# Kernel tuning notes

Measured on AMD Instinct MI355X. Metric: run time of the kernel, lower is better.

The kernel has to match this reference:

```python
import jax, jax.numpy as jnp
import numpy as np

DIM, H, D, B, L = 1024, 8, 64, 1, 256


def silu(v):
    return v * jax.nn.sigmoid(v)


def setup_inputs() -> dict:
    key = jax.random.key(0)
    ks = jax.random.split(key, 12)
    n = lambda i, shape, scale=1.0: jax.random.normal(ks[i], shape, dtype=jnp.float32) * scale
    return {
        "x": n(0, (B, L, DIM)),
        "hidden_real": n(1, (B, H, D)),
        "hidden_imag": n(2, (B, H, D)),
        "w_in1": n(3, (DIM, DIM), 1.0 / np.sqrt(DIM)),
        "b_in1": jnp.zeros((DIM,), jnp.float32),
        "w_in2": n(4, (DIM, H * D * 4), 1.0 / np.sqrt(DIM)),
        "b_in2": jnp.zeros((H * D * 4,), jnp.float32),
        "w_out1": n(5, (H * D * 2, DIM), 1.0 / np.sqrt(H * D * 2)),
        "b_out1": jnp.zeros((DIM,), jnp.float32),
        "w_out2": n(6, (DIM, DIM), 1.0 / np.sqrt(DIM)),
        "b_out2": jnp.zeros((DIM,), jnp.float32),
        "mat_v_real": n(7, (H, D, D)),
        "mat_v_imag": n(8, (H, D, D)),
    }


def reference(x, hidden_real, hidden_imag, w_in1, b_in1, w_in2, b_in2,
              w_out1, b_out1, w_out2, b_out2, mat_v_real, mat_v_imag):
    batch, slen, _ = x.shape
    t = silu(x @ w_in1 + b_in1)
    t = t @ w_in2 + b_in2                       # (B, L, 4*H*D)
    z = t.reshape(batch, slen, H, D, 2, 2)      # [..., {x,a}, {re,im}]
    xc = jax.lax.complex(z[..., 0, 0], z[..., 0, 1])   # (B, L, H, D) complex
    ac = jax.lax.complex(z[..., 1, 0], z[..., 1, 1])

    # normalize a: unit phase * sigmoid(log(|a|^2)) magnitude
    mag2 = ac.real * ac.real + ac.imag * ac.imag
    ac = ac * (jax.lax.rsqrt(mag2) * jax.nn.sigmoid(jnp.log(mag2)))

    a_ln = jnp.log(ac)                          # (B, L, H, D) complex
    al = jnp.transpose(a_ln, (0, 2, 3, 1))      # (B, H, D, L)

    # triu-broadcast + cumsum along cols == the FFT conv-with-ones in the original
    idx = jnp.arange(slen)
    triu = idx[:, None] <= idx[None, :]          # row i, col j: keep j >= i
    tri = jnp.where(triu, al[..., None, :], 0.0)  # (B, H, D, L, L)
    cum = jnp.cumsum(tri, axis=-1)               # cum[i, k] = sum_{j=i..k} a_ln[j]
    keep = (idx[:, None] - 1) <= idx[None, :]    # triu(diagonal=-1)
    c = jnp.where(keep, jnp.exp(cum), 0.0)       # c[i,k] = prod_{j=i..k} a[j]; c[i,i-1]=1

    V = jax.lax.complex(mat_v_real, mat_v_imag)  # (H, D, D)
    Vinv = jnp.linalg.inv(V)
    hidden = jax.lax.complex(hidden_real, hidden_imag)  # (B, H, D)

    x_roll = jnp.concatenate([hidden.astype(xc.dtype)[:, None], xc[:, :-1]], axis=1)
    u = jnp.einsum('hno,blho->blhn', Vinv, x_roll)       # V^{-1} applied per head
    h = jnp.einsum('bholm,blho->bmho', c, u)             # banded product-scan
    h = h.at[:, -1].add(jnp.einsum('hno,bho->bhn', Vinv, xc[:, -1]))
    h = jnp.einsum('hno,blho->blhn', V, h)               # back to V-basis

    hidden_next = h[:, -1]                                # (B, H, D) complex
    hr = jnp.stack([h.real, h.imag], axis=-1).reshape(batch, slen, H * D * 2)
    y = silu(hr @ w_out1 + b_out1)
    y = y @ w_out2 + b_out2
    return y, hidden_next
```

## Files before the change

kernel.cpp:

```cpp
#include <hip/hip_runtime.h>
#include <math.h>

#define DIMN 1024
#define NH 8
#define ND 64
#define LSEQ 256
#define HD 512

typedef __attribute__((ext_vector_type(8))) short short8;
typedef __attribute__((ext_vector_type(4))) float f32x4;

__device__ __forceinline__ float2 cmul(float2 a, float2 b){
    return make_float2(a.x*b.x - a.y*b.y, a.x*b.y + a.y*b.x);
}
__device__ __forceinline__ ushort f2bf(float f){
    union { float f; unsigned u; } v; v.f = f;
    unsigned r = v.u + 0x7FFF + ((v.u >> 16) & 1);
    return (ushort)(r >> 16);
}

#define ISTR 65
#define ASTR 40
#define BK 32

__device__ __forceinline__ void inv_gj_blocked(const float* __restrict__ Vr,
        const float* __restrict__ Vi, float2* __restrict__ Vinv,
        int h, int tid, float2* Mx){
    for (int idx = tid; idx < 4096; idx += 512){
        int i = idx >> 6, j = idx & 63;
        Mx[i*ISTR + j] = make_float2(Vr[h*4096 + idx], Vi[h*4096 + idx]);
    }
    __syncthreads();
    const int w = tid >> 6, l = tid & 63;
    const int rbase = w*8;
    for (int kb = 0; kb < 8; ++kb){
        const int k0 = kb*8;
        if (w == 0){
            float2 pr[8];
            #pragma unroll
            for (int m = 0; m < 8; ++m) pr[m] = Mx[l*ISTR + k0 + m];
            #pragma unroll
            for (int k = 0; k < 8; ++k){
                const int gk = k0 + k;
                float2 d; d.x = __shfl(pr[k].x, gk); d.y = __shfl(pr[k].y, gk);
                float im = 1.f/(d.x*d.x + d.y*d.y);
                float2 p = make_float2(d.x*im, -d.y*im);
                float2 spr[8];
                #pragma unroll
                for (int m = 0; m < 8; ++m){
                    float2 t; t.x = __shfl(pr[m].x, gk); t.y = __shfl(pr[m].y, gk);
                    spr[m] = (m == k) ? p : cmul(t, p);
                }
                float2 f = pr[k];
                if (l == gk){
                    #pragma unroll
                    for (int m = 0; m < 8; ++m) pr[m] = spr[m];
                } else {
                    #pragma unroll
                    for (int m = 0; m < 8; ++m){
                        float2 u = cmul(f, spr[m]);
                        if (m == k){ pr[m].x = -u.x;  pr[m].y = -u.y;  }
                        else       { pr[m].x -= u.x;  pr[m].y -= u.y;  }
                    }
                }
            }
            #pragma unroll
            for (int m = 0; m < 8; ++m) Mx[l*ISTR + k0 + m] = pr[m];
        }
        __syncthreads();
        float2 br[8];
        #pragma unroll
        for (int m = 0; m < 8; ++m) br[m] = Mx[(k0+m)*ISTR + l];
        __syncthreads();
        if (((unsigned)(l - k0)) >= 8u){
            #pragma unroll
            for (int rr = 0; rr < 8; ++rr){
                const int r = rbase + rr;
                float2 acc;
                if (((unsigned)(r - k0)) < 8u){ acc.x = 0.f; acc.y = 0.f; }
                else acc = Mx[r*ISTR + l];
                #pragma unroll
                for (int m = 0; m < 8; ++m){
                    float2 Pv = Mx[r*ISTR + k0 + m];
                    acc.x += Pv.x*br[m].x - Pv.y*br[m].y;
                    acc.y += Pv.x*br[m].y + Pv.y*br[m].x;
                }
                Mx[r*ISTR + l] = acc;
            }
        }
        __syncthreads();
    }
    for (int idx = tid; idx < 4096; idx += 512){
        int i = idx >> 6, j = idx & 63;
        Vinv[h*4096 + idx] = Mx[i*ISTR + j];
    }
}

__device__ __forceinline__ void w3eff_tile(const float* __restrict__ Vr,
        const float* __restrict__ Vi, const float* __restrict__ w3,
        ushort* __restrict__ W3bt, int t, int tid, float* lds){
    const int n0 = (t & 31)*32;
    const int c0 = (t >> 5)*32;
    const int h  = c0 >> 7;
    const int og0 = (c0 & 127) >> 1;
    float* Vbr = lds;
    float* Vbi = lds + 1024;
    float* Wb  = lds + 2048;
    for (int q = tid; q < 1024; q += 512){
        int dd = q >> 4, oo = q & 15;
        Vbr[q] = Vr[(h*64+dd)*64 + og0 + oo];
        Vbi[q] = Vi[(h*64+dd)*64 + og0 + oo];
    }
    for (int q = tid; q < 4096; q += 512){
        int row = q >> 5, nn = q & 31;
        Wb[q] = w3[(h*128 + row)*1024 + n0 + nn];
    }
    __syncthreads();
    const int nn = tid & 31, oo = tid >> 5;
    float ar = 0.f, ai = 0.f;
    #pragma unroll 8
    for (int dd = 0; dd < 64; ++dd){
        float vr = Vbr[dd*16 + oo], vi = Vbi[dd*16 + oo];
        float w0 = Wb[(dd*2)*32 + nn], w1v = Wb[(dd*2+1)*32 + nn];
        ar += vr*w0 + vi*w1v;
        ai += -vi*w0 + vr*w1v;
    }
    W3bt[(n0+nn)*1024 + c0 + oo*2 + 0] = f2bf(ar);
    W3bt[(n0+nn)*1024 + c0 + oo*2 + 1] = f2bf(ai);
}

__device__ __forceinline__ void gemm1_direct_tile(const float* __restrict__ x,
        const float* __restrict__ w1, const float* __restrict__ bias,
        ushort* __restrict__ Cb, int tile, int tid8, ushort* lds){
    ushort* As = lds;
    ushort* Bs = lds + 64*ASTR;
    const int bm = (tile & 3)*64, bn = (tile >> 2)*64;
    const int wave = tid8 >> 6, l = tid8 & 63;
    const int wr = (wave >> 1)*32, wc = (wave & 1)*32;
    const int ml = l & 15, quad = l >> 4;
    f32x4 acc[2][2];
    #pragma unroll
    for (int i=0;i<2;++i)
        #pragma unroll
        for (int j=0;j<2;++j) acc[i][j] = (f32x4){0.f,0.f,0.f,0.f};
    const int c0r = tid8 >> 2, c0s = tid8 & 3;
    const int bn_n = tid8 & 63, bk0 = (tid8 >> 6)*8;
    for (int k0 = 0; k0 < DIMN; k0 += BK){
        float4 a0 = *(const float4*)&x[(bm+c0r)*DIMN + k0 + c0s*8];
        float4 a1 = *(const float4*)&x[(bm+c0r)*DIMN + k0 + c0s*8 + 4];
        float bv[8];
        #pragma unroll
        for (int kk = 0; kk < 8; ++kk)
            bv[kk] = w1[(k0 + bk0 + kk)*DIMN + bn + bn_n];
        __syncthreads();
        ushort4 u0; u0.x=f2bf(a0.x); u0.y=f2bf(a0.y); u0.z=f2bf(a0.z); u0.w=f2bf(a0.w);
        ushort4 u1; u1.x=f2bf(a1.x); u1.y=f2bf(a1.y); u1.z=f2bf(a1.z); u1.w=f2bf(a1.w);
        *(ushort4*)&As[c0r*ASTR + c0s*8]     = u0;
        *(ushort4*)&As[c0r*ASTR + c0s*8 + 4] = u1;
        #pragma unroll
        for (int kk = 0; kk < 8; ++kk)
            Bs[bn_n*ASTR + bk0 + kk] = f2bf(bv[kk]);
        __syncthreads();
        short8 af[2], bfv[2];
        #pragma unroll
        for (int f=0; f<2; ++f){
            af[f]  = *(const short8*)&As[(wr + f*16 + ml)*ASTR + quad*8];
            bfv[f] = *(const short8*)&Bs[(wc + f*16 + ml)*ASTR + quad*8];
        }
        #pragma unroll
        for (int i=0;i<2;++i)
            #pragma unroll
            for (int j=0;j<2;++j)
                acc[i][j] = __builtin_amdgcn_mfma_f32_16x16x32_bf16(af[i], bfv[j], acc[i][j], 0,0,0);
    }
    #pragma unroll
    for (int i=0;i<2;++i){
        #pragma unroll
        for (int j=0;j<2;++j){
            const int gcol = bn + wc + j*16 + ml;
            const float bsv = bias[gcol];
            #pragma unroll
            for (int r=0;r<4;++r){
                const int grow = bm + wr + i*16 + quad*4 + r;
                float val = acc[i][j][r] + bsv;
                val *= 1.f/(1.f + expf(-val));
                Cb[grow*DIMN + gcol] = f2bf(val);
            }
        }
    }
}

__global__ __launch_bounds__(512) void mix1_kernel(
        const float* __restrict__ x,
        const float* __restrict__ w1, const float* __restrict__ w2,
        const float* __restrict__ w3, const float* __restrict__ w4,
        const float* __restrict__ Vr, const float* __restrict__ Vi,
        const float* __restrict__ b1,
        ushort* __restrict__ t1_bf,
        ushort* __restrict__ w2t, ushort* __restrict__ W3bt,
        ushort* __restrict__ w4t, float2* __restrict__ Vinv){
    __shared__ __align__(16) char lds_raw[33280];
    const int b = blockIdx.x;
    const int tid = threadIdx.x;
    const int half = tid >> 8;

    if (b < 32){
        gemm1_direct_tile(x, w1, b1, t1_bf, b*2 + half, tid & 255,
                          (ushort*)lds_raw + half*(128*ASTR));
        return;
    }
    if (b < 40){
        inv_gj_blocked(Vr, Vi, Vinv, b - 32, tid, (float2*)lds_raw);
        return;
    }
    int widx = b - 40;
    if (widx >= 1536){
        w3eff_tile(Vr, Vi, w3, W3bt, widx - 1536, tid, (float*)lds_raw);
        return;
    }
    const float* W; ushort* Wt; int K = 1024, N;
    if (widx < 1024){ W = w2; Wt = w2t; N = 2048; }
    else            { W = w4; Wt = w4t; N = 1024; widx -= 1024; }
    const int t = widx*2 + half;
    const int tiles_n = N >> 5;
    const int n0 = (t % tiles_n) * 32, k0 = (t / tiles_n) * 32;
    float* tile = (float*)lds_raw + half*(32*33);
    const int tx = tid & 31, ty = (tid >> 5) & 7;
    #pragma unroll
    for (int i = 0; i < 4; ++i)
        tile[(ty + i*8)*33 + tx] = W[(k0 + ty + i*8)*N + n0 + tx];
    __syncthreads();
    #pragma unroll
    for (int i = 0; i < 4; ++i){
        int r = ty + i*8;
        Wt[(n0 + r)*K + k0 + tx] = f2bf(tile[tx*33 + r]);
    }
}

__global__ __launch_bounds__(512) void inv_kernel(const float* __restrict__ Vr,
                                                  const float* __restrict__ Vi,
                                                  float2* __restrict__ Vinv){
    __shared__ float2 Mx[64*ISTR];
    inv_gj_blocked(Vr, Vi, Vinv, blockIdx.x, threadIdx.x, Mx);
}

__global__ __launch_bounds__(256) void transpose_cvt(const float* __restrict__ W,
                 ushort* __restrict__ Wt, int K, int N){
    __shared__ float tile[32][33];
    const int n0 = blockIdx.x * 32, k0 = blockIdx.y * 32;
    const int tx = threadIdx.x & 31, ty = threadIdx.x >> 5;
    #pragma unroll
    for (int i = 0; i < 4; ++i)
        tile[ty + i*8][tx] = W[(k0 + ty + i*8)*N + n0 + tx];
    __syncthreads();
    #pragma unroll
    for (int i = 0; i < 4; ++i){
        int r = ty + i*8;
        Wt[(n0 + r)*K + k0 + tx] = f2bf(tile[tx][r]);
    }
}

__global__ __launch_bounds__(256) void cvt_bf16_kernel(const float* __restrict__ in,
                                 ushort* __restrict__ o, int n4){
    int i = blockIdx.x*256 + threadIdx.x;
    if (i < n4){
        float4 v = ((const float4*)in)[i];
        ushort4 u; u.x=f2bf(v.x); u.y=f2bf(v.y); u.z=f2bf(v.z); u.w=f2bf(v.w);
        ((ushort4*)o)[i] = u;
    }
}

#define BM 64
#define BN 64
template<int ACT>
__global__ __launch_bounds__(256) void gemm_bt(const ushort* __restrict__ A,
                 const ushort* __restrict__ Bt, const float* __restrict__ bias,
                 float* __restrict__ Cf, ushort* __restrict__ Cb,
                 float2* __restrict__ XCo, float2* __restrict__ Ao,
                 int M, int N, int K,
                 const float* __restrict__ tVr, const float* __restrict__ tVi,
                 const float2* __restrict__ S255, float* __restrict__ out_tail,
                 int tail_n){
    __shared__ ushort As[BM*ASTR];
    __shared__ ushort Bs[BN*ASTR];
    const int tid = threadIdx.x;
    const int bm = blockIdx.y * BM, bn = blockIdx.x * BN;
    const int wave = tid >> 6, l = tid & 63;
    const int wr = (wave >> 1) * 32, wc = (wave & 1) * 32;
    const int ml = l & 15, quad = l >> 4;

    if (ACT == 0 && out_tail != nullptr && blockIdx.x == 0 && blockIdx.y == 0){
        for (int hn = tid; hn < 512; hn += 256){
            int h = hn >> 6;
            float2 acc2 = make_float2(0.f, 0.f);
            #pragma unroll 8
            for (int o = 0; o < 64; ++o){
                float2 v = make_float2(tVr[hn*64+o], tVi[hn*64+o]);
                float2 p = cmul(v, S255[h*64+o]);
                acc2.x += p.x; acc2.y += p.y;
            }
            if (tail_n >= 1024){
                out_tail[hn]       = acc2.x;
                out_tail[512 + hn] = acc2.y;
            } else if (tail_n >= 512){
                out_tail[hn] = acc2.x;
            }
        }
    }

    f32x4 acc[2][2];
    #pragma unroll
    for (int i=0;i<2;++i)
        #pragma unroll
        for (int j=0;j<2;++j) acc[i][j] = (f32x4){0.f,0.f,0.f,0.f};
    const int c0r = tid >> 2;
    const int c0s = tid & 3;
    for (int k0 = 0; k0 < K; k0 += BK){
        uint4 av = *(const uint4*)&A [(bm + c0r)*K + k0 + c0s*8];
        uint4 bv = *(const uint4*)&Bt[(bn + c0r)*K + k0 + c0s*8];
        __syncthreads();
        *(uint4*)&As[c0r*ASTR + c0s*8] = av;
        *(uint4*)&Bs[c0r*ASTR + c0s*8] = bv;
        __syncthreads();
        short8 af[2], bfv[2];
        #pragma unroll
        for (int f=0; f<2; ++f){
            af[f]  = *(const short8*)&As[(wr + f*16 + ml)*ASTR + quad*8];
            bfv[f] = *(const short8*)&Bs[(wc + f*16 + ml)*ASTR + quad*8];
        }
        #pragma unroll
        for (int i=0;i<2;++i)
            #pragma unroll
            for (int j=0;j<2;++j)
                acc[i][j] = __builtin_amdgcn_mfma_f32_16x16x32_bf16(af[i], bfv[j], acc[i][j], 0,0,0);
    }
    #pragma unroll
    for (int i=0;i<2;++i){
        #pragma unroll
        for (int j=0;j<2;++j){
            const int gcol = bn + wc + j*16 + ml;
            const float bsv = bias[gcol];
            #pragma unroll
            for (int r=0;r<4;++r){
                const int grow = bm + wr + i*16 + quad*4 + r;
                float val = acc[i][j][r] + bsv;
                if (ACT == 2){
                    float v1 = __shfl_down(val, 1);
                    float v2 = __shfl_down(val, 2);
                    float v3 = __shfl_down(val, 3);
                    if ((l & 3) == 0){
                        int hd = gcol >> 2;
                        XCo[grow*HD + hd] = make_float2(val, v1);
                        float m2 = v2*v2 + v3*v3;
                        float s = sqrtf(m2)/(1.f + m2);
                        Ao[grow*HD + hd] = make_float2(v2*s, v3*s);
                    }
                } else if (ACT == 1){
                    val *= 1.f/(1.f + expf(-val));
                    Cb[grow*N + gcol] = f2bf(val);
                } else {
                    Cf[grow*N + gcol] = val;
                }
            }
        }
    }
}

__global__ __launch_bounds__(512) void upscan_kernel(const float2* __restrict__ Vinv,
        const float* __restrict__ hidr, const float* __restrict__ him,
        const float2* __restrict__ XC, const float2* __restrict__ Aseq,
        ushort* __restrict__ Sb, float2* __restrict__ S255){
    __shared__ float4 buf[2][2][LSEQ];
    __shared__ float2 vrow[2][64];
    __shared__ float2 inu[2];
    const int b = blockIdx.x;
    const int tid = threadIdx.x;
    const int g = tid >> 8, m = tid & 255;
    const int hn = b*2 + g;
    const int h = hn >> 6;
    if (m < 64) vrow[g][m] = Vinv[hn*64 + m];
    __syncthreads();
    float2 acc = make_float2(0.f, 0.f);
    const float2* xrow = &XC[m*HD + h*64];
    #pragma unroll 8
    for (int o=0;o<64;++o){
        float2 p = cmul(vrow[g][o], xrow[o]);
        acc.x += p.x; acc.y += p.y;
    }
    if (m == 0){
        float2 i0 = make_float2(0.f, 0.f);
        #pragma unroll 8
        for (int o=0;o<64;++o){
            float2 hv = make_float2(hidr[h*64+o], him[h*64+o]);
            float2 p = cmul(vrow[g][o], hv);
            i0.x += p.x; i0.y += p.y;
        }
        inu[g] = i0;
    }
    float2 a = Aseq[m*HD + hn];
    buf[0][g][m] = make_float4(a.x, a.y, acc.x, acc.y);
    __syncthreads();
    int pb = 0;
    #pragma unroll
    for (int d = 1; d < LSEQ; d <<= 1){
        float4 cur = buf[pb][g][m];
        float4 o2 = cur;
        if (m >= d){
            float4 prev = buf[pb][g][m-d];
            float2 cA = make_float2(cur.x, cur.y), cU = make_float2(cur.z, cur.w);
            float2 pA = make_float2(prev.x, prev.y), pU = make_float2(prev.z, prev.w);
            float2 nA = cmul(cA, pA);
            float2 nU = cmul(cA, pU);
            nU.x += cU.x; nU.y += cU.y;
            o2 = make_float4(nA.x, nA.y, nU.x, nU.y);
        }
        buf[pb^1][g][m] = o2;
        pb ^= 1;
        __syncthreads();
    }
    float4 t = buf[pb][g][m];
    float2 init = inu[g];
    float2 st = cmul(make_float2(t.x, t.y), init);
    st.x += t.z; st.y += t.w;
    Sb[m*DIMN + hn*2]   = f2bf(st.x);
    Sb[m*DIMN + hn*2+1] = f2bf(st.y);
    if (m == LSEQ-1) S255[hn] = st;
}

__global__ __launch_bounds__(256) void vmul_kernel(const float* __restrict__ Vr,
                            const float* __restrict__ Vi,
                            const float2* __restrict__ S, ushort* __restrict__ hrb,
                            float* __restrict__ out_tail, int tail_n){
    int g = blockIdx.x*256 + threadIdx.x;
    int m = g >> 9, hn = g & 511;
    int h = hn >> 6;
    const float* vr = &Vr[hn*64];
    const float* vi = &Vi[hn*64];
    const float2* srow = &S[m*HD + h*64];
    float2 acc = make_float2(0.f, 0.f);
    #pragma unroll 8
    for (int o=0;o<64;++o){
        float2 v = make_float2(vr[o], vi[o]);
        float2 p = cmul(v, srow[o]);
        acc.x += p.x; acc.y += p.y;
    }
    hrb[m*DIMN + hn*2]   = f2bf(acc.x);
    hrb[m*DIMN + hn*2+1] = f2bf(acc.y);
    if (m == LSEQ-1){
        if (tail_n >= 1024){
            out_tail[hn]       = acc.x;
            out_tail[512 + hn] = acc.y;
        } else if (tail_n >= 512){
            out_tail[hn] = acc.x;
        }
    }
}

__global__ __launch_bounds__(512) void upscan_f32_kernel(const float2* __restrict__ Vinv,
        const float* __restrict__ hidr, const float* __restrict__ him,
        const float2* __restrict__ XC, const float2* __restrict__ Aseq,
        float2* __restrict__ S){
    __shared__ float4 buf[2][2][LSEQ];
    __shared__ float2 vrow[2][64];
    __shared__ float2 inu[2];
    const int b = blockIdx.x;
    const int tid = threadIdx.x;
    const int g = tid >> 8, m = tid & 255;
    const int hn = b*2 + g;
    const int h = hn >> 6;
    if (m < 64) vrow[g][m] = Vinv[hn*64 + m];
    __syncthreads();
    float2 acc = make_float2(0.f, 0.f);
    const float2* xrow = &XC[m*HD + h*64];
    #pragma unroll 8
    for (int o=0;o<64;++o){
        float2 p = cmul(vrow[g][o], xrow[o]);
        acc.x += p.x; acc.y += p.y;
    }
    if (m == 0){
        float2 i0 = make_float2(0.f, 0.f);
        #pragma unroll 8
        for (int o=0;o<64;++o){
            float2 hv = make_float2(hidr[h*64+o], him[h*64+o]);
            float2 p = cmul(vrow[g][o], hv);
            i0.x += p.x; i0.y += p.y;
        }
        inu[g] = i0;
    }
    float2 a = Aseq[m*HD + hn];
    buf[0][g][m] = make_float4(a.x, a.y, acc.x, acc.y);
    __syncthreads();
    int pb = 0;
    #pragma unroll
    for (int d = 1; d < LSEQ; d <<= 1){
        float4 cur = buf[pb][g][m];
        float4 o2 = cur;
        if (m >= d){
            float4 prev = buf[pb][g][m-d];
            float2 cA = make_float2(cur.x, cur.y), cU = make_float2(cur.z, cur.w);
            float2 pA = make_float2(prev.x, prev.y), pU = make_float2(prev.z, prev.w);
            float2 nA = cmul(cA, pA);
            float2 nU = cmul(cA, pU);
            nU.x += cU.x; nU.y += cU.y;
            o2 = make_float4(nA.x, nA.y, nU.x, nU.y);
        }
        buf[pb^1][g][m] = o2;
        pb ^= 1;
        __syncthreads();
    }
    float4 t = buf[pb][g][m];
    float2 init = inu[g];
    float2 st = cmul(make_float2(t.x, t.y), init);
    st.x += t.z; st.y += t.w;
    S[m*HD + hn] = st;
}

extern "C" void kernel_launch(void* const* d_in, const int* in_sizes, int n_in,
                              void* d_out, int out_size, void* d_ws, size_t ws_size,
                              hipStream_t stream) {
    const float* x      = (const float*)d_in[0];
    const float* hidr   = (const float*)d_in[1];
    const float* hidi   = (const float*)d_in[2];
    const float* w_in1  = (const float*)d_in[3];
    const float* b_in1  = (const float*)d_in[4];
    const float* w_in2  = (const float*)d_in[5];
    const float* b_in2  = (const float*)d_in[6];
    const float* w_out1 = (const float*)d_in[7];
    const float* b_out1 = (const float*)d_in[8];
    const float* w_out2 = (const float*)d_in[9];
    const float* b_out2 = (const float*)d_in[10];
    const float* Vr     = (const float*)d_in[11];
    const float* Vi     = (const float*)d_in[12];
    float* out = (float*)d_out;
    const int tail_n = out_size - LSEQ*DIMN;
    char* ws = (char*)d_ws;

    if (ws_size >= 14946304u){
        float2* Vinv  = (float2*)(ws + 0);
        ushort* w2t   = (ushort*)(ws + 2359296);
        ushort* W3bt  = (ushort*)(ws + 6553600);
        ushort* w4t   = (ushort*)(ws + 8650752);
        ushort* y1_bf = (ushort*)(ws + 10747904);
        ushort* t1_bf = (ushort*)(ws + 11272192);
        float2* XC    = (float2*)(ws + 11796480);
        float2* Aseq  = (float2*)(ws + 12845056);
        float2* S255  = (float2*)(ws + 13893632);
        ushort* Sb    = t1_bf;

        mix1_kernel<<<2600, 512, 0, stream>>>(x, w_in1, w_in2, w_out1, w_out2,
                                              Vr, Vi, b_in1, t1_bf, w2t, W3bt, w4t, Vinv);
        gemm_bt<2><<<dim3(32,4), 256, 0, stream>>>(t1_bf, w2t, b_in2, nullptr, nullptr,
                XC, Aseq, LSEQ, 2048, DIMN, nullptr, nullptr, nullptr, nullptr, 0);
        upscan_kernel<<<256, 512, 0, stream>>>(Vinv, hidr, hidi, XC, Aseq, Sb, S255);
        gemm_bt<1><<<dim3(16,4), 256, 0, stream>>>(Sb, W3bt, b_out1, nullptr, y1_bf,
                nullptr, nullptr, LSEQ, DIMN, DIMN, nullptr, nullptr, nullptr, nullptr, 0);
        gemm_bt<0><<<dim3(16,4), 256, 0, stream>>>(y1_bf, w4t, b_out2, out, nullptr,
                nullptr, nullptr, LSEQ, DIMN, DIMN, Vr, Vi, S255, out + LSEQ*DIMN, tail_n);
    } else {
        float2* Vinv  = (float2*)(ws + 0);
        ushort* wt    = (ushort*)(ws + 262144);
        ushort* x_bf  = (ushort*)(ws + 4456448);
        ushort* t1_bf = (ushort*)(ws + 4980736);
        float2* XC    = (float2*)(ws + 5505024);
        float2* Aseq  = (float2*)(ws + 6553600);
        float2* S     = (float2*)(ws + 7602176);
        ushort* y1_bf = x_bf;
        ushort* hr_bf = t1_bf;

        inv_kernel<<<NH, 512, 0, stream>>>(Vr, Vi, Vinv);
        cvt_bf16_kernel<<<LSEQ*DIMN/4/256, 256, 0, stream>>>(x, x_bf, LSEQ*DIMN/4);
        transpose_cvt<<<dim3(32,32), 256, 0, stream>>>(w_in1, wt, DIMN, DIMN);
        gemm_bt<1><<<dim3(16,4), 256, 0, stream>>>(x_bf, wt, b_in1, nullptr, t1_bf,
                nullptr, nullptr, LSEQ, DIMN, DIMN, nullptr, nullptr, nullptr, nullptr, 0);
        transpose_cvt<<<dim3(64,32), 256, 0, stream>>>(w_in2, wt, DIMN, 2048);
        gemm_bt<2><<<dim3(32,4), 256, 0, stream>>>(t1_bf, wt, b_in2, nullptr, nullptr,
                XC, Aseq, LSEQ, 2048, DIMN, nullptr, nullptr, nullptr, nullptr, 0);
        upscan_f32_kernel<<<256, 512, 0, stream>>>(Vinv, hidr, hidi, XC, Aseq, S);
        vmul_kernel<<<LSEQ*HD/256, 256, 0, stream>>>(Vr, Vi, S, hr_bf, out + LSEQ*DIMN, tail_n);
        transpose_cvt<<<dim3(32,32), 256, 0, stream>>>(w_out1, wt, DIMN, DIMN);
        gemm_bt<1><<<dim3(16,4), 256, 0, stream>>>(hr_bf, wt, b_out1, nullptr, y1_bf,
                nullptr, nullptr, LSEQ, DIMN, DIMN, nullptr, nullptr, nullptr, nullptr, 0);
        transpose_cvt<<<dim3(32,32), 256, 0, stream>>>(w_out2, wt, DIMN, DIMN);
        gemm_bt<0><<<dim3(16,4), 256, 0, stream>>>(y1_bf, wt, b_out2, out, nullptr,
                nullptr, nullptr, LSEQ, DIMN, DIMN, nullptr, nullptr, nullptr, nullptr, 0);
    }
}
```

Measured before the change: 197.6 us.

## Replace LDS-tiled GEMMs with single-wave direct-load MFMA GEMM kernels

The first GEMM no longer runs fused inside the prep kernel. The prep kernel now transposes and converts w_in1 to bf16 and converts x to bf16, alongside the existing weight prep work. All four GEMMs move to a new gemm_dt kernel that uses one 64-thread wave per 32x32 tile, loads MFMA fragments straight from global memory with register double-buffering and no LDS, and remaps block indices for locality. The hidden_next tail computation moves from the last GEMM to an extra block of the third GEMM. This trades LDS staging for many small blocks that fill more CUs, at the cost of an extra kernel launch and uncached, redundant global reads.

```diff
diff --git a/kernel.cpp b/kernel.cpp
--- a/kernel.cpp
+++ b/kernel.cpp
@@ -129,111 +129,162 @@
     W3bt[(n0+nn)*1024 + c0 + oo*2 + 1] = f2bf(ai);
 }
 
-__device__ __forceinline__ void gemm1_direct_tile(const float* __restrict__ x,
-        const float* __restrict__ w1, const float* __restrict__ bias,
-        ushort* __restrict__ Cb, int tile, int tid8, ushort* lds){
-    ushort* As = lds;
-    ushort* Bs = lds + 64*ASTR;
-    const int bm = (tile & 3)*64, bn = (tile >> 2)*64;
-    const int wave = tid8 >> 6, l = tid8 & 63;
-    const int wr = (wave >> 1)*32, wc = (wave & 1)*32;
-    const int ml = l & 15, quad = l >> 4;
-    f32x4 acc[2][2];
-    #pragma unroll
-    for (int i=0;i<2;++i)
-        #pragma unroll
-        for (int j=0;j<2;++j) acc[i][j] = (f32x4){0.f,0.f,0.f,0.f};
-    const int c0r = tid8 >> 2, c0s = tid8 & 3;
-    const int bn_n = tid8 & 63, bk0 = (tid8 >> 6)*8;
-    for (int k0 = 0; k0 < DIMN; k0 += BK){
-        float4 a0 = *(const float4*)&x[(bm+c0r)*DIMN + k0 + c0s*8];
-        float4 a1 = *(const float4*)&x[(bm+c0r)*DIMN + k0 + c0s*8 + 4];
-        float bv[8];
-        #pragma unroll
-        for (int kk = 0; kk < 8; ++kk)
-            bv[kk] = w1[(k0 + bk0 + kk)*DIMN + bn + bn_n];
-        __syncthreads();
-        ushort4 u0; u0.x=f2bf(a0.x); u0.y=f2bf(a0.y); u0.z=f2bf(a0.z); u0.w=f2bf(a0.w);
-        ushort4 u1; u1.x=f2bf(a1.x); u1.y=f2bf(a1.y); u1.z=f2bf(a1.z); u1.w=f2bf(a1.w);
-        *(ushort4*)&As[c0r*ASTR + c0s*8]     = u0;
-        *(ushort4*)&As[c0r*ASTR + c0s*8 + 4] = u1;
-        #pragma unroll
-        for (int kk = 0; kk < 8; ++kk)
-            Bs[bn_n*ASTR + bk0 + kk] = f2bf(bv[kk]);
-        __syncthreads();
-        short8 af[2], bfv[2];
-        #pragma unroll
-        for (int f=0; f<2; ++f){
-            af[f]  = *(const short8*)&As[(wr + f*16 + ml)*ASTR + quad*8];
-            bfv[f] = *(const short8*)&Bs[(wc + f*16 + ml)*ASTR + quad*8];
-        }
-        #pragma unroll
-        for (int i=0;i<2;++i)
-            #pragma unroll
-            for (int j=0;j<2;++j)
-                acc[i][j] = __builtin_amdgcn_mfma_f32_16x16x32_bf16(af[i], bfv[j], acc[i][j], 0,0,0);
-    }
-    #pragma unroll
-    for (int i=0;i<2;++i){
-        #pragma unroll
-        for (int j=0;j<2;++j){
-            const int gcol = bn + wc + j*16 + ml;
-            const float bsv = bias[gcol];
-            #pragma unroll
-            for (int r=0;r<4;++r){
-                const int grow = bm + wr + i*16 + quad*4 + r;
-                float val = acc[i][j][r] + bsv;
-                val *= 1.f/(1.f + expf(-val));
-                Cb[grow*DIMN + gcol] = f2bf(val);
-            }
-        }
-    }
-}
-
-__global__ __launch_bounds__(512) void mix1_kernel(
+__global__ __launch_bounds__(512) void prep_kernel(
         const float* __restrict__ x,
         const float* __restrict__ w1, const float* __restrict__ w2,
         const float* __restrict__ w3, const float* __restrict__ w4,
         const float* __restrict__ Vr, const float* __restrict__ Vi,
-        const float* __restrict__ b1,
-        ushort* __restrict__ t1_bf,
-        ushort* __restrict__ w2t, ushort* __restrict__ W3bt,
-        ushort* __restrict__ w4t, float2* __restrict__ Vinv){
+        ushort* __restrict__ x_bf,
+        ushort* __restrict__ w1t, ushort* __restrict__ w2t,
+        ushort* __restrict__ w4t, ushort* __restrict__ W3bt,
+        float2* __restrict__ Vinv){
     __shared__ __align__(16) char lds_raw[33280];
     const int b = blockIdx.x;
     const int tid = threadIdx.x;
     const int half = tid >> 8;
 
-    if (b < 32){
-        gemm1_direct_tile(x, w1, b1, t1_bf, b*2 + half, tid & 255,
-                          (ushort*)lds_raw + half*(128*ASTR));
+    if (b < 8){
+        inv_gj_blocked(Vr, Vi, Vinv, b, tid, (float2*)lds_raw);
         return;
     }
-    if (b < 40){
-        inv_gj_blocked(Vr, Vi, Vinv, b - 32, tid, (float2*)lds_raw);
+    int u = b - 8;
+    if (u < 2048){
+        const float* W; ushort* Wt; const int K = 1024; int N; int t;
+        if (u < 512)      { W = w1; Wt = w1t; N = 1024; t = u*2 + half; }
+        else if (u < 1536){ W = w2; Wt = w2t; N = 2048; t = (u-512)*2 + half; }
+        else              { W = w4; Wt = w4t; N = 1024; t = (u-1536)*2 + half; }
+        const int tiles_n = N >> 5;
+        const int n0 = (t % tiles_n) * 32, k0 = (t / tiles_n) * 32;
+        float* tile = (float*)lds_raw + half*(32*33);
+        const int tx = tid & 31, ty = (tid >> 5) & 7;
+        #pragma unroll
+        for (int i = 0; i < 4; ++i)
+            tile[(ty + i*8)*33 + tx] = W[(k0 + ty + i*8)*N + n0 + tx];
+        __syncthreads();
+        #pragma unroll
+        for (int i = 0; i < 4; ++i){
+            int r = ty + i*8;
+            Wt[(n0 + r)*K + k0 + tx] = f2bf(tile[tx*33 + r]);
+        }
         return;
     }
-    int widx = b - 40;
-    if (widx >= 1536){
-        w3eff_tile(Vr, Vi, w3, W3bt, widx - 1536, tid, (float*)lds_raw);
+    u -= 2048;
+    if (u < 64){
+        const int base = (u*512 + tid)*2;
+        #pragma unroll
+        for (int j = 0; j < 2; ++j){
+            float4 v = ((const float4*)x)[base + j];
+            ushort4 uu; uu.x=f2bf(v.x); uu.y=f2bf(v.y); uu.z=f2bf(v.z); uu.w=f2bf(v.w);
+            ((ushort4*)x_bf)[base + j] = uu;
+        }
         return;
     }
-    const float* W; ushort* Wt; int K = 1024, N;
-    if (widx < 1024){ W = w2; Wt = w2t; N = 2048; }
-    else            { W = w4; Wt = w4t; N = 1024; widx -= 1024; }
-    const int t = widx*2 + half;
-    const int tiles_n = N >> 5;
-    const int n0 = (t % tiles_n) * 32, k0 = (t / tiles_n) * 32;
-    float* tile = (float*)lds_raw + half*(32*33);
-    const int tx = tid & 31, ty = (tid >> 5) & 7;
-    #pragma unroll
-    for (int i = 0; i < 4; ++i)
-        tile[(ty + i*8)*33 + tx] = W[(k0 + ty + i*8)*N + n0 + tx];
-    __syncthreads();
-    #pragma unroll
-    for (int i = 0; i < 4; ++i){
-        int r = ty + i*8;
-        Wt[(n0 + r)*K + k0 + tx] = f2bf(tile[tx*33 + r]);
+    u -= 64;
+    w3eff_tile(Vr, Vi, w3, W3bt, u, tid, (float*)lds_raw);
+}
+
+template<int ACT>
+__global__ __launch_bounds__(64) void gemm_dt(const ushort* __restrict__ A,
+                 const ushort* __restrict__ Bt, const float* __restrict__ bias,
+                 float* __restrict__ Cf, ushort* __restrict__ Cb,
+                 float2* __restrict__ XCo, float2* __restrict__ Ao,
+                 int M, int N, int K,
+                 const float* __restrict__ tVr, const float* __restrict__ tVi,
+                 const float2* __restrict__ S255, float* __restrict__ out_tail,
+                 int tail_n){
+    const int nt = (M >> 5) * (N >> 5);
+    const int b = blockIdx.x;
+    if (ACT == 1 && out_tail != nullptr && b >= nt){
+        const int l = threadIdx.x;
+        for (int hn = l; hn < 512; hn += 64){
+            const int h = hn >> 6;
+            float2 acc2 = make_float2(0.f, 0.f);
+            #pragma unroll 8
+            for (int o = 0; o < 64; ++o){
+                float2 v = make_float2(tVr[hn*64+o], tVi[hn*64+o]);
+                float2 p = cmul(v, S255[h*64+o]);
+                acc2.x += p.x; acc2.y += p.y;
+            }
+            if (tail_n >= 1024){
+                out_tail[hn]       = acc2.x;
+                out_tail[512 + hn] = acc2.y;
+            } else if (tail_n >= 512){
+                out_tail[hn] = acc2.x;
+            }
+        }
+        return;
+    }
+    const int cpx = nt >> 3;
+    const int t = (b & 7)*cpx + (b >> 3);
+    const int tm = M >> 5;
+    const int bm = (t % tm) * 32, bn = (t / tm) * 32;
+
+    const int l = threadIdx.x;
+    const int ml = l & 15, quad = l >> 4;
+    const ushort* Ap = A  + (bm + ml)*K + quad*8;
+    const ushort* Bp = Bt + (bn + ml)*K + quad*8;
+
+    f32x4 acc[2][2];
+    #pragma unroll
+    for (int i=0;i<2;++i)
+        #pragma unroll
+        for (int j=0;j<2;++j) acc[i][j] = (f32x4){0.f,0.f,0.f,0.f};
+
+    short8 ac[2], bc[2];
+    ac[0] = *(const short8*)(Ap);
+    ac[1] = *(const short8*)(Ap + 16*K);
+    bc[0] = *(const short8*)(Bp);
+    bc[1] = *(const short8*)(Bp + 16*K);
+
+    #pragma unroll 4
+    for (int k0 = 32; k0 < K; k0 += 32){
+        short8 an[2], bn2[2];
+        an[0]  = *(const short8*)(Ap + k0);
+        an[1]  = *(const short8*)(Ap + 16*K + k0);
+        bn2[0] = *(const short8*)(Bp + k0);
+        bn2[1] = *(const short8*)(Bp + 16*K + k0);
+        #pragma unroll
+        for (int i=0;i<2;++i)
+            #pragma unroll
+            for (int j=0;j<2;++j)
+                acc[i][j] = __builtin_amdgcn_mfma_f32_16x16x32_bf16(ac[i], bc[j], acc[i][j], 0,0,0);
+        ac[0]=an[0]; ac[1]=an[1]; bc[0]=bn2[0]; bc[1]=bn2[1];
+    }
+    #pragma unroll
+    for (int i=0;i<2;++i)
+        #pragma unroll
+        for (int j=0;j<2;++j)
+            acc[i][j] = __builtin_amdgcn_mfma_f32_16x16x32_bf16(ac[i], bc[j], acc[i][j], 0,0,0);
+
+    #pragma unroll
+    for (int i=0;i<2;++i){
+        #pragma unroll
+        for (int j=0;j<2;++j){
+            const int gcol = bn + j*16 + ml;
+            const float bsv = bias[gcol];
+            #pragma unroll
+            for (int r=0;r<4;++r){
+                const int grow = bm + i*16 + quad*4 + r;
+                float val = acc[i][j][r] + bsv;
+                if (ACT == 2){
+                    float v1 = __shfl_down(val, 1);
+                    float v2 = __shfl_down(val, 2);
+                    float v3 = __shfl_down(val, 3);
+                    if ((l & 3) == 0){
+                        int hd = gcol >> 2;
+                        XCo[grow*HD + hd] = make_float2(val, v1);
+                        float m2 = v2*v2 + v3*v3;
+                        float s = sqrtf(m2)/(1.f + m2);
+                        Ao[grow*HD + hd] = make_float2(v2*s, v3*s);
+                    }
+                } else if (ACT == 1){
+                    val *= 1.f/(1.f + expf(-val));
+                    Cb[grow*N + gcol] = f2bf(val);
+                } else {
+                    Cf[grow*N + gcol] = val;
+                }
+            }
+        }
     }
 }
 
@@ -537,25 +588,29 @@
 
     if (ws_size >= 14946304u){
         float2* Vinv  = (float2*)(ws + 0);
-        ushort* w2t   = (ushort*)(ws + 2359296);
-        ushort* W3bt  = (ushort*)(ws + 6553600);
-        ushort* w4t   = (ushort*)(ws + 8650752);
-        ushort* y1_bf = (ushort*)(ws + 10747904);
+        ushort* w2t   = (ushort*)(ws + 262144);
+        ushort* W3bt  = (ushort*)(ws + 4456448);
+        ushort* w4t   = (ushort*)(ws + 6553600);
+        ushort* w1t   = (ushort*)(ws + 8650752);
+        float2* XC    = (float2*)(ws + 8650752);
+        float2* Aseq  = (float2*)(ws + 9699328);
+        ushort* x_bf  = (ushort*)(ws + 10747904);
+        float2* S255  = (float2*)(ws + 10747904);
         ushort* t1_bf = (ushort*)(ws + 11272192);
-        float2* XC    = (float2*)(ws + 11796480);
-        float2* Aseq  = (float2*)(ws + 12845056);
-        float2* S255  = (float2*)(ws + 13893632);
+        ushort* y1_bf = (ushort*)(ws + 11796480);
         ushort* Sb    = t1_bf;
 
-        mix1_kernel<<<2600, 512, 0, stream>>>(x, w_in1, w_in2, w_out1, w_out2,
-                                              Vr, Vi, b_in1, t1_bf, w2t, W3bt, w4t, Vinv);
-        gemm_bt<2><<<dim3(32,4), 256, 0, stream>>>(t1_bf, w2t, b_in2, nullptr, nullptr,
+        prep_kernel<<<3144, 512, 0, stream>>>(x, w_in1, w_in2, w_out1, w_out2,
+                                              Vr, Vi, x_bf, w1t, w2t, w4t, W3bt, Vinv);
+        gemm_dt<1><<<256, 64, 0, stream>>>(x_bf, w1t, b_in1, nullptr, t1_bf,
+                nullptr, nullptr, LSEQ, DIMN, DIMN, nullptr, nullptr, nullptr, nullptr, 0);
+        gemm_dt<2><<<512, 64, 0, stream>>>(t1_bf, w2t, b_in2, nullptr, nullptr,
                 XC, Aseq, LSEQ, 2048, DIMN, nullptr, nullptr, nullptr, nullptr, 0);
         upscan_kernel<<<256, 512, 0, stream>>>(Vinv, hidr, hidi, XC, Aseq, Sb, S255);
-        gemm_bt<1><<<dim3(16,4), 256, 0, stream>>>(Sb, W3bt, b_out1, nullptr, y1_bf,
+        gemm_dt<1><<<257, 64, 0, stream>>>(Sb, W3bt, b_out1, nullptr, y1_bf,
+                nullptr, nullptr, LSEQ, DIMN, DIMN, Vr, Vi, S255, out + LSEQ*DIMN, tail_n);
+        gemm_dt<0><<<256, 64, 0, stream>>>(y1_bf, w4t, b_out2, out, nullptr,
                 nullptr, nullptr, LSEQ, DIMN, DIMN, nullptr, nullptr, nullptr, nullptr, 0);
-        gemm_bt<0><<<dim3(16,4), 256, 0, stream>>>(y1_bf, w4t, b_out2, out, nullptr,
-                nullptr, nullptr, LSEQ, DIMN, DIMN, Vr, Vi, S255, out + LSEQ*DIMN, tail_n);
     } else {
         float2* Vinv  = (float2*)(ws + 0);
         ushort* wt    = (ushort*)(ws + 262144);
```

After: 200.9 us. About the same (+1.7%).
